# Kernel tuning notes

Measured on AMD Instinct MI355X. Metric: run time of the kernel, lower is better.

Reference implementation:

```python
import jax, jax.numpy as jnp
import numpy as np

N_USER, N_PC, N_URL = 200000, 50000, 100000
E_USES, E_VISITS = 1000000, 1000000
H = 64
NUM_LAYERS = 2


def setup_inputs() -> dict:
    key = jax.random.key(0)
    ks = jax.random.split(key, 32)
    ki = iter(ks)

    def nrm(shape, scale=0.1):
        return jax.random.normal(next(ki), shape, dtype=jnp.float32) * scale

    inp = {
        "x_user": jax.random.normal(next(ki), (N_USER, 6), dtype=jnp.float32),
        "x_pc": jax.random.normal(next(ki), (N_PC, 4), dtype=jnp.float32),
        "x_url": jax.random.normal(next(ki), (N_URL, 3), dtype=jnp.float32),
        # edge_uses: row0 = user src ids, row1 = pc dst ids
        "edge_uses": jnp.stack([
            jax.random.randint(next(ki), (E_USES,), 0, N_USER),
            jax.random.randint(next(ki), (E_USES,), 0, N_PC),
        ]).astype(jnp.int32),
        # edge_visits: row0 = user src ids, row1 = url dst ids
        "edge_visits": jnp.stack([
            jax.random.randint(next(ki), (E_VISITS,), 0, N_USER),
            jax.random.randint(next(ki), (E_VISITS,), 0, N_URL),
        ]).astype(jnp.int32),
        # input projections (PyG Linear: y = x @ W + b)
        "Wu": nrm((6, H)), "bu": nrm((H,)),
        "Wp": nrm((4, H)), "bp": nrm((H,)),
        "Wl": nrm((3, H)), "bl": nrm((H,)),
        # per layer, per relation SAGEConv params; relation order:
        # 0: user-uses->pc, 1: pc-used_by->user, 2: user-visits->url, 3: url-visited_by->user
        "sage_l_W": nrm((NUM_LAYERS, 4, H, H)),
        "sage_l_b": nrm((NUM_LAYERS, 4, H)),
        "sage_r_W": nrm((NUM_LAYERS, 4, H, H)),
        # classifier (dropout is identity at eval)
        "cW1": nrm((H, H // 2)), "cb1": nrm((H // 2,)),
        "cW2": nrm((H // 2, 2)), "cb2": nrm((2,)),
    }
    return inp


def _sage(x_src, x_dst, src_idx, dst_idx, W_l, b_l, W_r, n_dst):
    # SAGEConv: lin_l(mean_{neighbors} x_src) + lin_r(x_dst)
    msg = x_src[src_idx]                                   # [E, H] gather
    s = jax.ops.segment_sum(msg, dst_idx, num_segments=n_dst)
    cnt = jax.ops.segment_sum(jnp.ones((src_idx.shape[0],), jnp.float32),
                              dst_idx, num_segments=n_dst)[:, None]
    mean = jnp.where(cnt > 0, s / jnp.maximum(cnt, 1.0), 0.0)
    return mean @ W_l + b_l + x_dst @ W_r


def reference(x_user, x_pc, x_url, edge_uses, edge_visits,
              Wu, bu, Wp, bp, Wl, bl,
              sage_l_W, sage_l_b, sage_r_W,
              cW1, cb1, cW2, cb2):
    hu = x_user @ Wu + bu
    hp = x_pc @ Wp + bp
    hl = x_url @ Wl + bl

    u2p_s, u2p_d = edge_uses[0], edge_uses[1]
    u2l_s, u2l_d = edge_visits[0], edge_visits[1]

    for layer in range(NUM_LAYERS):
        WL, BL, WR = sage_l_W[layer], sage_l_b[layer], sage_r_W[layer]
        new_pc = _sage(hu, hp, u2p_s, u2p_d, WL[0], BL[0], WR[0], N_PC)
        new_user = (_sage(hp, hu, u2p_d, u2p_s, WL[1], BL[1], WR[1], N_USER)
                    + _sage(hl, hu, u2l_d, u2l_s, WL[3], BL[3], WR[3], N_USER))
        new_url = _sage(hu, hl, u2l_s, u2l_d, WL[2], BL[2], WR[2], N_URL)
        hu, hp, hl = jax.nn.relu(new_user), jax.nn.relu(new_pc), jax.nn.relu(new_url)

    h = jax.nn.relu(hu @ cW1 + cb1)
    return h @ cW2 + cb2
```

## Files before the change

### kernel.cpp

```cpp
#include <hip/hip_runtime.h>

typedef __attribute__((ext_vector_type(8))) short bf16x8;
typedef __attribute__((ext_vector_type(4))) float f32x4;
typedef unsigned short u16;

constexpr int NUSER = 200000;
constexpr int NPC   = 50000;
constexpr int NURL  = 100000;
constexpr int EUSES = 1000000;
constexpr int EVIS  = 1000000;
constexpr int HD    = 64;

constexpr int SB_P  = 0;
constexpr int SB_U1 = NPC;
constexpr int SB_L  = NPC + NUSER;
constexpr int SB_U2 = NPC + NUSER + NURL;
constexpr int NTOT  = NPC + NUSER + NURL + NUSER;

constexpr int CAP_P = 56;
constexpr int CAP_U = 28;
constexpr int CAP_L = 36;

constexpr int NBIN  = 128;
constexpr int NBINS = 512;

__device__ __forceinline__ int binOfP(int k) { return (k * NBIN) / NPC; }
__device__ __forceinline__ int binOfU(int k) { return (k * NBIN) / NUSER; }
__device__ __forceinline__ int binOfL(int k) { return (k * NBIN) / NURL; }

__device__ __forceinline__ u16 f2bf(float f) {
    union { float f; unsigned u; } v; v.f = f;
    unsigned r = v.u + 0x7fff + ((v.u >> 16) & 1);
    return (u16)(r >> 16);
}
__device__ __forceinline__ float bf2f(u16 b) {
    union { unsigned u; float f; } v; v.u = ((unsigned)b) << 16; return v.f;
}
__device__ __forceinline__ void acc8(float* a, uint4 v) {
    unsigned w0 = v.x, w1 = v.y, w2 = v.z, w3 = v.w;
    a[0] += bf2f((u16)(w0 & 0xffff)); a[1] += bf2f((u16)(w0 >> 16));
    a[2] += bf2f((u16)(w1 & 0xffff)); a[3] += bf2f((u16)(w1 >> 16));
    a[4] += bf2f((u16)(w2 & 0xffff)); a[5] += bf2f((u16)(w2 >> 16));
    a[6] += bf2f((u16)(w3 & 0xffff)); a[7] += bf2f((u16)(w3 >> 16));
}


__global__ __launch_bounds__(256) void proj_k(
    const float* __restrict__ x, const float* __restrict__ W,
    const float* __restrict__ b, u16* __restrict__ h,
    int n, int din)
{
    int id = blockIdx.x * 256 + threadIdx.x;
    int node = id >> 6, c = id & 63;
    if (node >= n) return;
    float acc = b[c];
    for (int k = 0; k < din; ++k)
        acc += x[node * din + k] * W[k * 64 + c];
    h[id] = f2bf(acc);
}

__global__ __launch_bounds__(256) void bin_count_k(
    const int* __restrict__ eu, const int* __restrict__ ev,
    int* __restrict__ binCnt)
{
    __shared__ int hist[NBINS];
    int tid = threadIdx.x;
    for (int i = tid; i < NBINS; i += 256) hist[i] = 0;
    __syncthreads();
    int stride = gridDim.x * 256;
    for (int e = blockIdx.x * 256 + tid; e < EUSES; e += stride) {
        int s = __builtin_nontemporal_load(eu + e);
        int d = __builtin_nontemporal_load(eu + EUSES + e);
        atomicAdd(&hist[binOfP(d)], 1);
        atomicAdd(&hist[NBIN + binOfU(s)], 1);
    }
    for (int e = blockIdx.x * 256 + tid; e < EVIS; e += stride) {
        int s = __builtin_nontemporal_load(ev + e);
        int d = __builtin_nontemporal_load(ev + EVIS + e);
        atomicAdd(&hist[2 * NBIN + binOfL(d)], 1);
        atomicAdd(&hist[3 * NBIN + binOfU(s)], 1);
    }
    __syncthreads();
    for (int i = tid; i < NBINS; i += 256)
        if (hist[i]) atomicAdd(&binCnt[i], hist[i]);
}

__global__ __launch_bounds__(256) void bin_scan_k(
    const int* __restrict__ binCnt, int* __restrict__ binBase,
    int* __restrict__ binCursor)
{
    __shared__ int lds[256];
    int t = threadIdx.x;
    int carry = 0;
    for (int base = 0; base < NBINS; base += 256) {
        int v = binCnt[base + t];
        int x = v;
        lds[t] = x; __syncthreads();
        for (int off = 1; off < 256; off <<= 1) {
            int y = (t >= off) ? lds[t - off] : 0;
            __syncthreads();
            x += y; lds[t] = x;
            __syncthreads();
        }
        int excl = carry + x - v;
        binBase[base + t] = excl;
        binCursor[base + t] = excl;
        carry += lds[255];
        __syncthreads();
    }
}

__global__ __launch_bounds__(256) void bin_scatter_k(
    const int* __restrict__ eu, const int* __restrict__ ev,
    int* __restrict__ binCursor, int2* __restrict__ binned)
{
    __shared__ int hist[NBINS];
    __shared__ int base[NBINS];
    int tid = threadIdx.x;
    for (int i = tid; i < NBINS; i += 256) hist[i] = 0;
    __syncthreads();
    int stride = gridDim.x * 256;
    for (int e = blockIdx.x * 256 + tid; e < EUSES; e += stride) {
        int s = __builtin_nontemporal_load(eu + e);
        int d = __builtin_nontemporal_load(eu + EUSES + e);
        atomicAdd(&hist[binOfP(d)], 1);
        atomicAdd(&hist[NBIN + binOfU(s)], 1);
    }
    for (int e = blockIdx.x * 256 + tid; e < EVIS; e += stride) {
        int s = __builtin_nontemporal_load(ev + e);
        int d = __builtin_nontemporal_load(ev + EVIS + e);
        atomicAdd(&hist[2 * NBIN + binOfL(d)], 1);
        atomicAdd(&hist[3 * NBIN + binOfU(s)], 1);
    }
    __syncthreads();
    for (int i = tid; i < NBINS; i += 256)
        base[i] = hist[i] ? atomicAdd(&binCursor[i], hist[i]) : 0;
    __syncthreads();
    for (int i = tid; i < NBINS; i += 256) hist[i] = 0;
    __syncthreads();
    for (int e = blockIdx.x * 256 + tid; e < EUSES; e += stride) {
        int s = __builtin_nontemporal_load(eu + e);
        int d = __builtin_nontemporal_load(eu + EUSES + e);
        int b0 = binOfP(d);
        int r0 = atomicAdd(&hist[b0], 1);
        binned[(size_t)base[b0] + r0] = make_int2(d, s);
        int b1 = NBIN + binOfU(s);
        int r1 = atomicAdd(&hist[b1], 1);
        binned[(size_t)base[b1] + r1] = make_int2(s, d);
    }
    for (int e = blockIdx.x * 256 + tid; e < EVIS; e += stride) {
        int s = __builtin_nontemporal_load(ev + e);
        int d = __builtin_nontemporal_load(ev + EVIS + e);
        int b2 = 2 * NBIN + binOfL(d);
        int r2 = atomicAdd(&hist[b2], 1);
        binned[(size_t)base[b2] + r2] = make_int2(d, s);
        int b3 = 3 * NBIN + binOfU(s);
        int r3 = atomicAdd(&hist[b3], 1);
        binned[(size_t)base[b3] + r3] = make_int2(s, d);
    }
}

__global__ __launch_bounds__(256) void bucket_build_k(
    const int2* __restrict__ binned, const int* __restrict__ binBase,
    const int* __restrict__ binCnt, int* __restrict__ deg,
    int* __restrict__ colP, int* __restrict__ colU1,
    int* __restrict__ colL, int* __restrict__ colU2)
{
    __shared__ int ldsDeg[1568];
    int bin = blockIdx.x;
    int rel = bin >> 7, sub = bin & (NBIN - 1);
    int tid = threadIdx.x;
    int range, slot0, cap;
    int* col;
    if (rel == 0)      { range = NPC;   slot0 = SB_P;  col = colP;  cap = CAP_P; }
    else if (rel == 1) { range = NUSER; slot0 = SB_U1; col = colU1; cap = CAP_U; }
    else if (rel == 2) { range = NURL;  slot0 = SB_L;  col = colL;  cap = CAP_L; }
    else               { range = NUSER; slot0 = SB_U2; col = colU2; cap = CAP_U; }
    int lo = (sub * range + NBIN - 1) / NBIN;
    int hi = ((sub + 1) * range + NBIN - 1) / NBIN;
    int nk = hi - lo;
    for (int i = tid; i < nk; i += 256) ldsDeg[i] = 0;
    __syncthreads();
    int b0 = binBase[bin], cnt = binCnt[bin];
    for (int i = tid; i < cnt; i += 256) {
        int2 kp = binned[(size_t)b0 + i];
        int r = atomicAdd(&ldsDeg[kp.x - lo], 1);
        if (r < cap) col[(size_t)kp.x * cap + r] = kp.y;
    }
    __syncthreads();
    for (int i = tid; i < nk; i += 256) deg[slot0 + lo + i] = ldsDeg[i];
}

__global__ __launch_bounds__(256) void gather_all_k(
    const u16* __restrict__ hu, const u16* __restrict__ hp,
    const u16* __restrict__ hl,
    const int* __restrict__ colP, const int* __restrict__ colU1,
    const int* __restrict__ colL, const int* __restrict__ colU2,
    const int* __restrict__ deg, u16* __restrict__ meanAll)
{
    int t = blockIdx.x * 256 + threadIdx.x;
    int slot = t >> 3;
    if (slot >= NTOT) return;
    int lane = (t & 7) << 3;
    const u16* hsrc;
    const int* col;
    int cap;
    if (slot < SB_U1)      { hsrc = hu; col = colP  + (size_t)(slot)         * CAP_P; cap = CAP_P; }
    else if (slot < SB_L)  { hsrc = hp; col = colU1 + (size_t)(slot - SB_U1) * CAP_U; cap = CAP_U; }
    else if (slot < SB_U2) { hsrc = hu; col = colL  + (size_t)(slot - SB_L)  * CAP_L; cap = CAP_L; }
    else                   { hsrc = hl; col = colU2 + (size_t)(slot - SB_U2) * CAP_U; cap = CAP_U; }
    int dg = deg[slot];
    int m_n = dg < cap ? dg : cap;
    float a[8] = {0.f,0.f,0.f,0.f,0.f,0.f,0.f,0.f};
    int j = 0;
    for (; j + 4 <= m_n; j += 4) {
        int c0 = __builtin_nontemporal_load(col + j);
        int c1 = __builtin_nontemporal_load(col + j + 1);
        int c2 = __builtin_nontemporal_load(col + j + 2);
        int c3 = __builtin_nontemporal_load(col + j + 3);
        uint4 v0 = *(const uint4*)(hsrc + (size_t)c0 * 64 + lane);
        uint4 v1 = *(const uint4*)(hsrc + (size_t)c1 * 64 + lane);
        uint4 v2 = *(const uint4*)(hsrc + (size_t)c2 * 64 + lane);
        uint4 v3 = *(const uint4*)(hsrc + (size_t)c3 * 64 + lane);
        acc8(a, v0); acc8(a, v1); acc8(a, v2); acc8(a, v3);
    }
    for (; j < m_n; ++j) {
        int c = __builtin_nontemporal_load(col + j);
        uint4 v = *(const uint4*)(hsrc + (size_t)c * 64 + lane);
        acc8(a, v);
    }
    float inv = dg > 0 ? 1.f / (float)dg : 0.f;
    uint4 m;
    m.x = (unsigned)f2bf(a[0] * inv) | ((unsigned)f2bf(a[1] * inv) << 16);
    m.y = (unsigned)f2bf(a[2] * inv) | ((unsigned)f2bf(a[3] * inv) << 16);
    m.z = (unsigned)f2bf(a[4] * inv) | ((unsigned)f2bf(a[5] * inv) << 16);
    m.w = (unsigned)f2bf(a[6] * inv) | ((unsigned)f2bf(a[7] * inv) << 16);
    *(uint4*)(meanAll + (size_t)slot * 64 + lane) = m;
}

__global__ __launch_bounds__(256) void btprep_k(
    const float* __restrict__ lW, const float* __restrict__ lB,
    const float* __restrict__ rW,
    u16* __restrict__ bt, float* __restrict__ bias)
{
    int idx = blockIdx.x * 256 + threadIdx.x;
    if (idx < 57344) {
        int layer = idx / 28672, rem = idx % 28672;
        size_t wb = (size_t)layer * 4 * 4096;
        int n, k, K; float val; u16* out;
        if (rem < 8192) {
            K = 128; n = rem >> 7; k = rem & 127;
            val = k < 64 ? lW[wb + 0 * 4096 + k * 64 + n]
                         : rW[wb + 0 * 4096 + (k - 64) * 64 + n];
            out = bt + (size_t)layer * 28672;
        } else if (rem < 16384) {
            int e = rem - 8192; K = 128; n = e >> 7; k = e & 127;
            val = k < 64 ? lW[wb + 2 * 4096 + k * 64 + n]
                         : rW[wb + 2 * 4096 + (k - 64) * 64 + n];
            out = bt + (size_t)layer * 28672 + 8192;
        } else {
            int e = rem - 16384; K = 192; n = e / 192; k = e % 192;
            if (k < 64)       val = lW[wb + 1 * 4096 + k * 64 + n];
            else if (k < 128) val = lW[wb + 3 * 4096 + (k - 64) * 64 + n];
            else              val = rW[wb + 1 * 4096 + (k - 128) * 64 + n]
                                  + rW[wb + 3 * 4096 + (k - 128) * 64 + n];
            out = bt + (size_t)layer * 28672 + 16384;
        }
        int byte = n * (2 * K) + 2 * k;
        byte ^= ((n & 7) << 4);
        out[byte >> 1] = f2bf(val);
    } else if (idx < 57728) {
        int i2 = idx - 57344;
        int layer = i2 / 192, r = i2 % 192, which = r / 64, c = r % 64;
        size_t bb = (size_t)layer * 4 * 64;
        float v;
        if (which == 0)      v = lB[bb + 0 * 64 + c];
        else if (which == 1) v = lB[bb + 2 * 64 + c];
        else                 v = lB[bb + 1 * 64 + c] + lB[bb + 3 * 64 + c];
        bias[(layer * 3 + which) * 64 + c] = v;
    }
}

template<int STEPS>
__global__ __launch_bounds__(256) void sage_mfma_k(
    const u16* __restrict__ src0, const u16* __restrict__ src1,
    const u16* __restrict__ src2, u16* __restrict__ hout,
    const u16* __restrict__ Bt, const float* __restrict__ bias, int n)
{
    constexpr int K = STEPS * 32;
    __shared__ u16 sB[64 * K];
    int tid = threadIdx.x;
    for (int i = tid; i < 64 * K / 8; i += 256)
        ((uint4*)sB)[i] = ((const uint4*)Bt)[i];
    __syncthreads();

    int lane = tid & 63, wave = tid >> 6;
    int row0 = blockIdx.x * 64 + wave * 16;
    int arow = row0 + (lane & 15);
    int kq = (lane >> 4) * 8;
    bool rowok = arow < n;

    const u16* srcs[3] = {src0, src1, src2};
    f32x4 acc0 = {0.f,0.f,0.f,0.f}, acc1 = acc0, acc2 = acc0, acc3 = acc0;
    f32x4* acc[4] = {&acc0, &acc1, &acc2, &acc3};

    #pragma unroll
    for (int s = 0; s < STEPS; ++s) {
        const u16* sp = srcs[s >> 1];
        int klocal = (s & 1) * 32 + kq;
        bf16x8 afrag = {0,0,0,0,0,0,0,0};
        if (rowok) afrag = *(const bf16x8*)(sp + (size_t)arow * 64 + klocal);
        int kk = s * 32 + kq;
        #pragma unroll
        for (int t = 0; t < 4; ++t) {
            int colc = t * 16 + (lane & 15);
            int byte = colc * (2 * K) + kk * 2;
            byte ^= ((colc & 7) << 4);
            bf16x8 bfrag = *(const bf16x8*)((const char*)sB + byte);
            *acc[t] = __builtin_amdgcn_mfma_f32_16x16x32_bf16(afrag, bfrag, *acc[t], 0, 0, 0);
        }
    }

    #pragma unroll
    for (int t = 0; t < 4; ++t) {
        int colc = t * 16 + (lane & 15);
        float bs = bias[colc];
        #pragma unroll
        for (int r = 0; r < 4; ++r) {
            int row = row0 + (lane >> 4) * 4 + r;
            if (row < n)
                hout[(size_t)row * 64 + colc] = f2bf(fmaxf((*acc[t])[r] + bs, 0.f));
        }
    }
}

__global__ __launch_bounds__(256) void classifier_k(
    const u16* __restrict__ hu,
    const float* __restrict__ cW1, const float* __restrict__ cb1,
    const float* __restrict__ cW2, const float* __restrict__ cb2,
    float* __restrict__ out, int n)
{
    __shared__ float sW1[64 * 32];
    __shared__ float sX[32][65];
    __shared__ float sHid[32][33];
    __shared__ float sW2[64];
    __shared__ float sb1[32];
    __shared__ float sb2[2];
    int tid = threadIdx.x;
    for (int i = tid; i < 2048; i += 256) sW1[i] = cW1[i];
    if (tid < 64) sW2[tid] = cW2[tid];
    if (tid < 32) sb1[tid] = cb1[tid];
    if (tid < 2)  sb2[tid] = cb2[tid];
    int row0 = blockIdx.x * 32;
    {
        int r = tid >> 3, k8 = (tid & 7) * 8;
        int gr = row0 + r;
        if (gr < n) {
            uint4 v = *(const uint4*)(hu + (size_t)gr * 64 + k8);
            unsigned w[4] = {v.x, v.y, v.z, v.w};
            #pragma unroll
            for (int j = 0; j < 4; ++j) {
                sX[r][k8 + 2 * j]     = bf2f((u16)(w[j] & 0xffff));
                sX[r][k8 + 2 * j + 1] = bf2f((u16)(w[j] >> 16));
            }
        } else {
            #pragma unroll
            for (int j = 0; j < 8; ++j) sX[r][k8 + j] = 0.f;
        }
    }
    __syncthreads();
    int c  = tid & 31;
    int rb = tid >> 5;
    for (int r = rb; r < 32; r += 8) {
        float acc = sb1[c];
        #pragma unroll
        for (int k = 0; k < 64; ++k) acc += sX[r][k] * sW1[k * 32 + c];
        sHid[r][c] = fmaxf(acc, 0.f);
    }
    __syncthreads();
    if (tid < 64) {
        int r = tid >> 1, j = tid & 1;
        int gr = row0 + r;
        if (gr < n) {
            float acc = sb2[j];
            #pragma unroll
            for (int k = 0; k < 32; ++k) acc += sHid[r][k] * sW2[k * 2 + j];
            out[gr * 2 + j] = acc;
        }
    }
}

extern "C" void kernel_launch(void* const* d_in, const int* in_sizes, int n_in,
                              void* d_out, int out_size, void* d_ws, size_t ws_size,
                              hipStream_t stream)
{
    const float* x_user = (const float*)d_in[0];
    const float* x_pc   = (const float*)d_in[1];
    const float* x_url  = (const float*)d_in[2];
    const int*   e_uses = (const int*)d_in[3];
    const int*   e_vis  = (const int*)d_in[4];
    const float* Wu = (const float*)d_in[5];
    const float* bu = (const float*)d_in[6];
    const float* Wp = (const float*)d_in[7];
    const float* bp = (const float*)d_in[8];
    const float* Wl = (const float*)d_in[9];
    const float* bl = (const float*)d_in[10];
    const float* sage_l_W = (const float*)d_in[11];
    const float* sage_l_b = (const float*)d_in[12];
    const float* sage_r_W = (const float*)d_in[13];
    const float* cW1 = (const float*)d_in[14];
    const float* cb1 = (const float*)d_in[15];
    const float* cW2 = (const float*)d_in[16];
    const float* cb2 = (const float*)d_in[17];
    float* out = (float*)d_out;

    char* p = (char*)d_ws;
    auto alloc = [&](size_t bytes) { char* r = p; p += (bytes + 255) & ~(size_t)255; return r; };
    u16* hu      = (u16*)alloc((size_t)NUSER * HD * 2);
    u16* hp      = (u16*)alloc((size_t)NPC * HD * 2);
    u16* hl      = (u16*)alloc((size_t)NURL * HD * 2);
    u16* meanAll = (u16*)alloc((size_t)NTOT * HD * 2);
    u16* btbuf   = (u16*)alloc((size_t)2 * 28672 * 2);
    float* biasbuf = (float*)alloc((size_t)2 * 3 * 64 * 4);
    int* deg     = (int*)alloc((size_t)NTOT * 4);
    int* colP    = (int*)alloc((size_t)NPC   * CAP_P * 4);
    int* colU1   = (int*)alloc((size_t)NUSER * CAP_U * 4);
    int* colL    = (int*)alloc((size_t)NURL  * CAP_L * 4);
    int* colU2   = (int*)alloc((size_t)NUSER * CAP_U * 4);
    int* binCnt    = (int*)alloc(NBINS * 4);
    int* binBase   = (int*)alloc(NBINS * 4);
    int* binCursor = (int*)alloc(NBINS * 4);
    int2* binned   = (int2*)alloc((size_t)2 * (EUSES + EVIS) * 8);

    u16* meanP  = meanAll + (size_t)SB_P  * HD;
    u16* meanU1 = meanAll + (size_t)SB_U1 * HD;
    u16* meanL  = meanAll + (size_t)SB_L  * HD;
    u16* meanU2 = meanAll + (size_t)SB_U2 * HD;

    hipMemsetAsync(binCnt, 0, NBINS * sizeof(int), stream);
    bin_count_k<<<256, 256, 0, stream>>>(e_uses, e_vis, binCnt);
    bin_scan_k<<<1, 256, 0, stream>>>(binCnt, binBase, binCursor);
    bin_scatter_k<<<256, 256, 0, stream>>>(e_uses, e_vis, binCursor, binned);
    bucket_build_k<<<NBINS, 256, 0, stream>>>(
        binned, binBase, binCnt, deg, colP, colU1, colL, colU2);

    btprep_k<<<(57728 + 255) / 256, 256, 0, stream>>>(
        sage_l_W, sage_l_b, sage_r_W, btbuf, biasbuf);
    proj_k<<<(NUSER * 64 + 255) / 256, 256, 0, stream>>>(x_user, Wu, bu, hu, NUSER, 6);
    proj_k<<<(NPC   * 64 + 255) / 256, 256, 0, stream>>>(x_pc,   Wp, bp, hp, NPC,   4);
    proj_k<<<(NURL  * 64 + 255) / 256, 256, 0, stream>>>(x_url,  Wl, bl, hl, NURL,  3);

    for (int layer = 0; layer < 2; ++layer) {
        const u16* btP = btbuf + (size_t)layer * 28672;
        const u16* btL = btP + 8192;
        const u16* btU = btP + 16384;
        const float* bsP = biasbuf + (layer * 3 + 0) * 64;
        const float* bsL = biasbuf + (layer * 3 + 1) * 64;
        const float* bsU = biasbuf + (layer * 3 + 2) * 64;

        gather_all_k<<<(NTOT * 8 + 255) / 256, 256, 0, stream>>>(
            hu, hp, hl, colP, colU1, colL, colU2, deg, meanAll);

        sage_mfma_k<4><<<(NPC + 63) / 64, 256, 0, stream>>>(
            meanP, hp, hp, hp, btP, bsP, NPC);
        sage_mfma_k<4><<<(NURL + 63) / 64, 256, 0, stream>>>(
            meanL, hl, hl, hl, btL, bsL, NURL);
        sage_mfma_k<6><<<(NUSER + 63) / 64, 256, 0, stream>>>(
            meanU1, meanU2, hu, hu, btU, bsU, NUSER);
    }

    classifier_k<<<(NUSER + 31) / 32, 256, 0, stream>>>(
        hu, cW1, cb1, cW2, cb2, out, NUSER);
}
```

Baseline: 528.8 us.

## Fuse neighbor-mean gather into SAGE MFMA kernel via LDS, ping-pong feature buffers

Replaces the separate gather kernel and three per-type MFMA kernels with one fused kernel per layer. Each block gathers neighbor means for its 64 destination rows directly into shared memory and then runs the MFMA projection from LDS, so the intermediate mean buffer is never written to or read back from global memory. Ping-pong feature buffers are needed because the fused kernel reads old features while writing new ones. Weights are now read straight from global memory without the LDS staging and swizzle, which may add cache traffic in exchange for fewer launches.

Result: slower. 563.4 us (+6.5%).

```diff
diff --git a/kernel.cpp b/kernel.cpp
--- a/kernel.cpp
+++ b/kernel.cpp
@@ -24,6 +24,11 @@
 constexpr int NBIN  = 128;
 constexpr int NBINS = 512;
 
+constexpr int NBLK_P = (NPC + 63) / 64;
+constexpr int NBLK_L = (NURL + 63) / 64;
+constexpr int NBLK_U = (NUSER + 63) / 64;
+constexpr int NBLK_TOT = NBLK_P + NBLK_L + NBLK_U;
+
 __device__ __forceinline__ int binOfP(int k) { return (k * NBIN) / NPC; }
 __device__ __forceinline__ int binOfU(int k) { return (k * NBIN) / NUSER; }
 __device__ __forceinline__ int binOfL(int k) { return (k * NBIN) / NURL; }
@@ -42,6 +47,38 @@
     a[2] += bf2f((u16)(w1 & 0xffff)); a[3] += bf2f((u16)(w1 >> 16));
     a[4] += bf2f((u16)(w2 & 0xffff)); a[5] += bf2f((u16)(w2 >> 16));
     a[6] += bf2f((u16)(w3 & 0xffff)); a[7] += bf2f((u16)(w3 >> 16));
+}
+
+__device__ __forceinline__ void gath8(
+    const u16* __restrict__ hsrc, const int* __restrict__ col,
+    int dg, int cap, int lane8, u16* dst)
+{
+    int m_n = dg < cap ? dg : cap;
+    float a[8] = {0.f,0.f,0.f,0.f,0.f,0.f,0.f,0.f};
+    int j = 0;
+    for (; j + 4 <= m_n; j += 4) {
+        int c0 = __builtin_nontemporal_load(col + j);
+        int c1 = __builtin_nontemporal_load(col + j + 1);
+        int c2 = __builtin_nontemporal_load(col + j + 2);
+        int c3 = __builtin_nontemporal_load(col + j + 3);
+        uint4 v0 = *(const uint4*)(hsrc + (size_t)c0 * 64 + lane8);
+        uint4 v1 = *(const uint4*)(hsrc + (size_t)c1 * 64 + lane8);
+        uint4 v2 = *(const uint4*)(hsrc + (size_t)c2 * 64 + lane8);
+        uint4 v3 = *(const uint4*)(hsrc + (size_t)c3 * 64 + lane8);
+        acc8(a, v0); acc8(a, v1); acc8(a, v2); acc8(a, v3);
+    }
+    for (; j < m_n; ++j) {
+        int c = __builtin_nontemporal_load(col + j);
+        uint4 v = *(const uint4*)(hsrc + (size_t)c * 64 + lane8);
+        acc8(a, v);
+    }
+    float inv = dg > 0 ? 1.f / (float)dg : 0.f;
+    uint4 m;
+    m.x = (unsigned)f2bf(a[0] * inv) | ((unsigned)f2bf(a[1] * inv) << 16);
+    m.y = (unsigned)f2bf(a[2] * inv) | ((unsigned)f2bf(a[3] * inv) << 16);
+    m.z = (unsigned)f2bf(a[4] * inv) | ((unsigned)f2bf(a[5] * inv) << 16);
+    m.w = (unsigned)f2bf(a[6] * inv) | ((unsigned)f2bf(a[7] * inv) << 16);
+    *(uint4*)dst = m;
 }
 
 
@@ -189,53 +226,6 @@
     }
     __syncthreads();
     for (int i = tid; i < nk; i += 256) deg[slot0 + lo + i] = ldsDeg[i];
-}
-
-__global__ __launch_bounds__(256) void gather_all_k(
-    const u16* __restrict__ hu, const u16* __restrict__ hp,
-    const u16* __restrict__ hl,
-    const int* __restrict__ colP, const int* __restrict__ colU1,
-    const int* __restrict__ colL, const int* __restrict__ colU2,
-    const int* __restrict__ deg, u16* __restrict__ meanAll)
-{
-    int t = blockIdx.x * 256 + threadIdx.x;
-    int slot = t >> 3;
-    if (slot >= NTOT) return;
-    int lane = (t & 7) << 3;
-    const u16* hsrc;
-    const int* col;
-    int cap;
-    if (slot < SB_U1)      { hsrc = hu; col = colP  + (size_t)(slot)         * CAP_P; cap = CAP_P; }
-    else if (slot < SB_L)  { hsrc = hp; col = colU1 + (size_t)(slot - SB_U1) * CAP_U; cap = CAP_U; }
-    else if (slot < SB_U2) { hsrc = hu; col = colL  + (size_t)(slot - SB_L)  * CAP_L; cap = CAP_L; }
-    else                   { hsrc = hl; col = colU2 + (size_t)(slot - SB_U2) * CAP_U; cap = CAP_U; }
-    int dg = deg[slot];
-    int m_n = dg < cap ? dg : cap;
-    float a[8] = {0.f,0.f,0.f,0.f,0.f,0.f,0.f,0.f};
-    int j = 0;
-    for (; j + 4 <= m_n; j += 4) {
-        int c0 = __builtin_nontemporal_load(col + j);
-        int c1 = __builtin_nontemporal_load(col + j + 1);
-        int c2 = __builtin_nontemporal_load(col + j + 2);
-        int c3 = __builtin_nontemporal_load(col + j + 3);
-        uint4 v0 = *(const uint4*)(hsrc + (size_t)c0 * 64 + lane);
-        uint4 v1 = *(const uint4*)(hsrc + (size_t)c1 * 64 + lane);
-        uint4 v2 = *(const uint4*)(hsrc + (size_t)c2 * 64 + lane);
-        uint4 v3 = *(const uint4*)(hsrc + (size_t)c3 * 64 + lane);
-        acc8(a, v0); acc8(a, v1); acc8(a, v2); acc8(a, v3);
-    }
-    for (; j < m_n; ++j) {
-        int c = __builtin_nontemporal_load(col + j);
-        uint4 v = *(const uint4*)(hsrc + (size_t)c * 64 + lane);
-        acc8(a, v);
-    }
-    float inv = dg > 0 ? 1.f / (float)dg : 0.f;
-    uint4 m;
-    m.x = (unsigned)f2bf(a[0] * inv) | ((unsigned)f2bf(a[1] * inv) << 16);
-    m.y = (unsigned)f2bf(a[2] * inv) | ((unsigned)f2bf(a[3] * inv) << 16);
-    m.z = (unsigned)f2bf(a[4] * inv) | ((unsigned)f2bf(a[5] * inv) << 16);
-    m.w = (unsigned)f2bf(a[6] * inv) | ((unsigned)f2bf(a[7] * inv) << 16);
-    *(uint4*)(meanAll + (size_t)slot * 64 + lane) = m;
 }
 
 __global__ __launch_bounds__(256) void btprep_k(
@@ -266,9 +256,7 @@
                                   + rW[wb + 3 * 4096 + (k - 128) * 64 + n];
             out = bt + (size_t)layer * 28672 + 16384;
         }
-        int byte = n * (2 * K) + 2 * k;
-        byte ^= ((n & 7) << 4);
-        out[byte >> 1] = f2bf(val);
+        out[n * K + k] = f2bf(val);
     } else if (idx < 57728) {
         int i2 = idx - 57344;
         int layer = i2 / 192, r = i2 % 192, which = r / 64, c = r % 64;
@@ -282,56 +270,90 @@
 }
 
 template<int STEPS>
-__global__ __launch_bounds__(256) void sage_mfma_k(
-    const u16* __restrict__ src0, const u16* __restrict__ src1,
-    const u16* __restrict__ src2, u16* __restrict__ hout,
-    const u16* __restrict__ Bt, const float* __restrict__ bias, int n)
+__device__ __forceinline__ void mfma_body(
+    const u16 (*sM)[136], const u16* __restrict__ xsrc,
+    const u16* __restrict__ Bt, const float* __restrict__ bs,
+    u16* __restrict__ hout, int row0, int n, int tid)
 {
     constexpr int K = STEPS * 32;
-    __shared__ u16 sB[64 * K];
-    int tid = threadIdx.x;
-    for (int i = tid; i < 64 * K / 8; i += 256)
-        ((uint4*)sB)[i] = ((const uint4*)Bt)[i];
-    __syncthreads();
-
     int lane = tid & 63, wave = tid >> 6;
-    int row0 = blockIdx.x * 64 + wave * 16;
-    int arow = row0 + (lane & 15);
+    int r_l = wave * 16 + (lane & 15);
+    int arow = row0 + r_l;
     int kq = (lane >> 4) * 8;
     bool rowok = arow < n;
-
-    const u16* srcs[3] = {src0, src1, src2};
-    f32x4 acc0 = {0.f,0.f,0.f,0.f}, acc1 = acc0, acc2 = acc0, acc3 = acc0;
-    f32x4* acc[4] = {&acc0, &acc1, &acc2, &acc3};
-
+    f32x4 acc[4] = {{0.f,0.f,0.f,0.f},{0.f,0.f,0.f,0.f},
+                    {0.f,0.f,0.f,0.f},{0.f,0.f,0.f,0.f}};
     #pragma unroll
     for (int s = 0; s < STEPS; ++s) {
-        const u16* sp = srcs[s >> 1];
-        int klocal = (s & 1) * 32 + kq;
         bf16x8 afrag = {0,0,0,0,0,0,0,0};
-        if (rowok) afrag = *(const bf16x8*)(sp + (size_t)arow * 64 + klocal);
-        int kk = s * 32 + kq;
+        if (s < STEPS - 2) {
+            afrag = *(const bf16x8*)(&sM[r_l][s * 32 + kq]);
+        } else if (rowok) {
+            afrag = *(const bf16x8*)(xsrc + (size_t)arow * 64 + (s - (STEPS - 2)) * 32 + kq);
+        }
         #pragma unroll
         for (int t = 0; t < 4; ++t) {
             int colc = t * 16 + (lane & 15);
-            int byte = colc * (2 * K) + kk * 2;
-            byte ^= ((colc & 7) << 4);
-            bf16x8 bfrag = *(const bf16x8*)((const char*)sB + byte);
-            *acc[t] = __builtin_amdgcn_mfma_f32_16x16x32_bf16(afrag, bfrag, *acc[t], 0, 0, 0);
-        }
-    }
-
+            bf16x8 bfrag = *(const bf16x8*)(Bt + colc * K + s * 32 + kq);
+            acc[t] = __builtin_amdgcn_mfma_f32_16x16x32_bf16(afrag, bfrag, acc[t], 0, 0, 0);
+        }
+    }
     #pragma unroll
     for (int t = 0; t < 4; ++t) {
         int colc = t * 16 + (lane & 15);
-        float bs = bias[colc];
+        float bsv = bs[colc];
         #pragma unroll
-        for (int r = 0; r < 4; ++r) {
-            int row = row0 + (lane >> 4) * 4 + r;
+        for (int rr = 0; rr < 4; ++rr) {
+            int row = row0 + wave * 16 + (lane >> 4) * 4 + rr;
             if (row < n)
-                hout[(size_t)row * 64 + colc] = f2bf(fmaxf((*acc[t])[r] + bs, 0.f));
-        }
-    }
+                hout[(size_t)row * 64 + colc] = f2bf(fmaxf(acc[t][rr] + bsv, 0.f));
+        }
+    }
+}
+
+__global__ __launch_bounds__(256) void sage_fused_k(
+    const u16* __restrict__ hu_o, const u16* __restrict__ hp_o,
+    const u16* __restrict__ hl_o,
+    u16* __restrict__ hu_n, u16* __restrict__ hp_n, u16* __restrict__ hl_n,
+    const int* __restrict__ colP, const int* __restrict__ colU1,
+    const int* __restrict__ colL, const int* __restrict__ colU2,
+    const int* __restrict__ deg,
+    const u16* __restrict__ bt, const float* __restrict__ bias)
+{
+    __shared__ u16 sM[64][136];
+    int bid = blockIdx.x, tid = threadIdx.x;
+    int seg, row0, n;
+    if (bid < NBLK_P)               { seg = 0; row0 = bid * 64;                      n = NPC; }
+    else if (bid < NBLK_P + NBLK_L) { seg = 1; row0 = (bid - NBLK_P) * 64;           n = NURL; }
+    else                            { seg = 2; row0 = (bid - NBLK_P - NBLK_L) * 64;  n = NUSER; }
+
+    int grow = tid >> 3;
+    int gl8 = (tid & 7) << 3;
+    for (int pass = 0; pass < 2; ++pass) {
+        int r = pass * 32 + grow;
+        int row = row0 + r;
+        bool ok = row < n;
+        if (seg == 0) {
+            gath8(hu_o, colP + (size_t)row * CAP_P, ok ? deg[SB_P + row] : 0,
+                  CAP_P, gl8, &sM[r][gl8]);
+        } else if (seg == 1) {
+            gath8(hu_o, colL + (size_t)row * CAP_L, ok ? deg[SB_L + row] : 0,
+                  CAP_L, gl8, &sM[r][gl8]);
+        } else {
+            gath8(hp_o, colU1 + (size_t)row * CAP_U, ok ? deg[SB_U1 + row] : 0,
+                  CAP_U, gl8, &sM[r][gl8]);
+            gath8(hl_o, colU2 + (size_t)row * CAP_U, ok ? deg[SB_U2 + row] : 0,
+                  CAP_U, gl8, &sM[r][64 + gl8]);
+        }
+    }
+    __syncthreads();
+
+    if (seg == 0)
+        mfma_body<4>(sM, hp_o, bt,         bias,       hp_n, row0, n, tid);
+    else if (seg == 1)
+        mfma_body<4>(sM, hl_o, bt + 8192,  bias + 64,  hl_n, row0, n, tid);
+    else
+        mfma_body<6>(sM, hu_o, bt + 16384, bias + 128, hu_n, row0, n, tid);
 }
 
 __global__ __launch_bounds__(256) void classifier_k(
@@ -416,10 +438,12 @@
 
     char* p = (char*)d_ws;
     auto alloc = [&](size_t bytes) { char* r = p; p += (bytes + 255) & ~(size_t)255; return r; };
-    u16* hu      = (u16*)alloc((size_t)NUSER * HD * 2);
-    u16* hp      = (u16*)alloc((size_t)NPC * HD * 2);
-    u16* hl      = (u16*)alloc((size_t)NURL * HD * 2);
-    u16* meanAll = (u16*)alloc((size_t)NTOT * HD * 2);
+    u16* huA = (u16*)alloc((size_t)NUSER * HD * 2);
+    u16* hpA = (u16*)alloc((size_t)NPC * HD * 2);
+    u16* hlA = (u16*)alloc((size_t)NURL * HD * 2);
+    u16* huB = (u16*)alloc((size_t)NUSER * HD * 2);
+    u16* hpB = (u16*)alloc((size_t)NPC * HD * 2);
+    u16* hlB = (u16*)alloc((size_t)NURL * HD * 2);
     u16* btbuf   = (u16*)alloc((size_t)2 * 28672 * 2);
     float* biasbuf = (float*)alloc((size_t)2 * 3 * 64 * 4);
     int* deg     = (int*)alloc((size_t)NTOT * 4);
@@ -432,11 +456,6 @@
     int* binCursor = (int*)alloc(NBINS * 4);
     int2* binned   = (int2*)alloc((size_t)2 * (EUSES + EVIS) * 8);
 
-    u16* meanP  = meanAll + (size_t)SB_P  * HD;
-    u16* meanU1 = meanAll + (size_t)SB_U1 * HD;
-    u16* meanL  = meanAll + (size_t)SB_L  * HD;
-    u16* meanU2 = meanAll + (size_t)SB_U2 * HD;
-
     hipMemsetAsync(binCnt, 0, NBINS * sizeof(int), stream);
     bin_count_k<<<256, 256, 0, stream>>>(e_uses, e_vis, binCnt);
     bin_scan_k<<<1, 256, 0, stream>>>(binCnt, binBase, binCursor);
@@ -446,29 +465,19 @@
 
     btprep_k<<<(57728 + 255) / 256, 256, 0, stream>>>(
         sage_l_W, sage_l_b, sage_r_W, btbuf, biasbuf);
-    proj_k<<<(NUSER * 64 + 255) / 256, 256, 0, stream>>>(x_user, Wu, bu, hu, NUSER, 6);
-    proj_k<<<(NPC   * 64 + 255) / 256, 256, 0, stream>>>(x_pc,   Wp, bp, hp, NPC,   4);
-    proj_k<<<(NURL  * 64 + 255) / 256, 256, 0, stream>>>(x_url,  Wl, bl, hl, NURL,  3);
-
-    for (int layer = 0; layer < 2; ++layer) {
-        const u16* btP = btbuf + (size_t)layer * 28672;
-        const u16* btL = btP + 8192;
-        const u16* btU = btP + 16384;
-        const float* bsP = biasbuf + (layer * 3 + 0) * 64;
-        const float* bsL = biasbuf + (layer * 3 + 1) * 64;
-        const float* bsU = biasbuf + (layer * 3 + 2) * 64;
-
-        gather_all_k<<<(NTOT * 8 + 255) / 256, 256, 0, stream>>>(
-            hu, hp, hl, colP, colU1, colL, colU2, deg, meanAll);
-
-        sage_mfma_k<4><<<(NPC + 63) / 64, 256, 0, stream>>>(
-            meanP, hp, hp, hp, btP, bsP, NPC);
-        sage_mfma_k<4><<<(NURL + 63) / 64, 256, 0, stream>>>(
-            meanL, hl, hl, hl, btL, bsL, NURL);
-        sage_mfma_k<6><<<(NUSER + 63) / 64, 256, 0, stream>>>(
-            meanU1, meanU2, hu, hu, btU, bsU, NUSER);
-    }
+    proj_k<<<(NUSER * 64 + 255) / 256, 256, 0, stream>>>(x_user, Wu, bu, huA, NUSER, 6);
+    proj_k<<<(NPC   * 64 + 255) / 256, 256, 0, stream>>>(x_pc,   Wp, bp, hpA, NPC,   4);
+    proj_k<<<(NURL  * 64 + 255) / 256, 256, 0, stream>>>(x_url,  Wl, bl, hlA, NURL,  3);
+
+    sage_fused_k<<<NBLK_TOT, 256, 0, stream>>>(
+        huA, hpA, hlA, huB, hpB, hlB,
+        colP, colU1, colL, colU2, deg,
+        btbuf, biasbuf);
+    sage_fused_k<<<NBLK_TOT, 256, 0, stream>>>(
+        huB, hpB, hlB, huA, hpA, hlA,
+        colP, colU1, colL, colU2, deg,
+        btbuf + 28672, biasbuf + 3 * 64);
 
     classifier_k<<<(NUSER + 31) / 32, 256, 0, stream>>>(
-        hu, cW1, cb1, cW2, cb2, out, NUSER);
-}
+        huA, cW1, cb1, cW2, cb2, out, NUSER);
+}
```
